# Kernel optimization log

Hardware: AMD Instinct MI355X
Metric: run time of the kernel (lower is better)

The kernel has to match this reference:

```python
import jax, jax.numpy as jnp
import numpy as np

ALPHA = 0.2  # LeakyReLU slope
NEG_INF = -9e15


def setup_inputs() -> dict:
    key = jax.random.key(0)
    ks = jax.random.split(key, 10)
    N, K, d = 20000, 32, 128
    R, S = 100, 4  # num relations, num domains
    item_embs = jax.random.normal(ks[0], (N, d), dtype=jnp.float32)
    entity_embs = jax.random.normal(ks[1], (N, K, d), dtype=jnp.float32)
    relations_embed = jax.random.normal(ks[2], (N, K, d), dtype=jnp.float32)
    relation_ids = jax.random.randint(ks[3], (N, K), 0, R, dtype=jnp.int32)
    adj_mask = jax.random.randint(ks[4], (N, K), 0, 2, dtype=jnp.int32)
    # fc_attention: Linear(3d, 1); out: Linear(d, d)
    fc_w = jax.random.normal(ks[5], (1, 3 * d), dtype=jnp.float32) * (1.0 / np.sqrt(3 * d))
    fc_b = jnp.zeros((1,), dtype=jnp.float32)
    out_w = jax.random.normal(ks[6], (d, d), dtype=jnp.float32) * (1.0 / np.sqrt(d))
    out_b = jnp.zeros((d,), dtype=jnp.float32)
    rel_dom_probs = jax.nn.softmax(jax.random.normal(ks[7], (R, S), dtype=jnp.float32), axis=-1)
    return {"item_embs": item_embs, "entity_embs": entity_embs,
            "relations_embed": relations_embed, "relation_ids": relation_ids,
            "adj_mask": adj_mask, "fc_w": fc_w, "fc_b": fc_b,
            "out_w": out_w, "out_b": out_b, "rel_dom_probs": rel_dom_probs}


def reference(item_embs, entity_embs, relations_embed, relation_ids, adj_mask,
              fc_w, fc_b, out_w, out_b, rel_dom_probs):
    N, K, d = entity_embs.shape
    R = rel_dom_probs.shape[0]
    # edge attention score: Linear(3d,1) on [item | relation | entity], then LeakyReLU
    Wh = jnp.broadcast_to(item_embs[:, None, :], (N, K, d))
    att_in = jnp.concatenate([Wh, relations_embed, entity_embs], axis=-1)  # [N,K,3d]
    e = jnp.einsum('nkf,of->nk', att_in, fc_w) + fc_b[0]
    e = jnp.where(e > 0, e, ALPHA * e)
    # masked softmax over neighbors (dropout inert in eval)
    masked = jnp.where(adj_mask > 0, e, NEG_INF)
    pi = jax.nn.softmax(masked, axis=1)  # [N,K]
    base = pi[..., None] * relations_embed * entity_embs  # [N,K,d]
    # domain-weighted aggregation: sum_s probs[rel_id, s], invalid ids -> 0
    valid = (relation_ids >= 0) & (relation_ids < R)
    safe_ids = jnp.clip(relation_ids, 0, R - 1)
    a_total = jnp.where(valid, rel_dom_probs[safe_ids].sum(-1), 0.0)  # [N,K]
    agg = jnp.einsum('nk,nkd->nd', a_total, base)  # [N,d]
    # residual + output Linear + ReLU
    out = (agg + item_embs) @ out_w.T + out_b
    return jax.nn.relu(out)
```

## Files before the change

kernel.cpp:

```cpp
#include <hip/hip_runtime.h>

#define ALPHA 0.2f

__device__ __forceinline__ float dot4(float4 a, float4 b) {
    return a.x * b.x + a.y * b.y + a.z * b.z + a.w * b.w;
}

__device__ __forceinline__ void block_bar() {
    asm volatile("s_waitcnt lgkmcnt(0)" ::: "memory");
    __builtin_amdgcn_s_barrier();
}

__global__ __launch_bounds__(256, 4)
void gat_k1(const float* __restrict__ item,
            const float* __restrict__ ent,
            const float* __restrict__ rel,
            const int*   __restrict__ rel_ids,
            const int*   __restrict__ adj,
            const float* __restrict__ fc_w,
            const float* __restrict__ fc_b,
            const float* __restrict__ probs,
            float* __restrict__ y,
            int N, int R)
{
    __shared__ float e_lds[32];
    __shared__ __align__(16) float part[4][128];
    __shared__ float asum[128];

    const int t  = threadIdx.x;
    const int w  = t >> 6;
    const int l  = t & 63;
    const int lh = l & 31;
    const int hi = l >> 5;
    const int kb = w * 8;

    for (int i = t; i < R; i += 256) {
        float4 q = *(const float4*)&probs[i * 4];
        asum[i] = q.x + q.y + q.z + q.w;
    }
    const float4 fi = *(const float4*)&fc_w[4 * lh];
    const float4 fr = *(const float4*)&fc_w[128 + 4 * lh];
    const float4 fe = *(const float4*)&fc_w[256 + 4 * lh];
    const float fcb = fc_b[0];
    __syncthreads();

    const int ST = gridDim.x;
    const int n0 = blockIdx.x;

    float4 rc[4], ec[4], itc;
    int adjc, idc;
    {
        const float* bR = rel + (size_t)n0 * 4096;
        const float* bE = ent + (size_t)n0 * 4096;
        #pragma unroll
        for (int c = 0; c < 4; ++c) {
            const int kk = kb + 2 * c + hi;
            rc[c] = *(const float4*)&bR[kk * 128 + 4 * lh];
            ec[c] = *(const float4*)&bE[kk * 128 + 4 * lh];
        }
        itc  = *(const float4*)&item[(size_t)n0 * 128 + 4 * lh];
        adjc = adj[(size_t)n0 * 32 + lh];
        idc  = rel_ids[(size_t)n0 * 32 + lh];
    }

    for (int n = n0; n < N; n += ST) {
        float4 p[4];
        float  ep[4];
        #pragma unroll
        for (int c = 0; c < 4; ++c) {
            p[c].x = rc[c].x * ec[c].x;
            p[c].y = rc[c].y * ec[c].y;
            p[c].z = rc[c].z * ec[c].z;
            p[c].w = rc[c].w * ec[c].w;
            ep[c]  = dot4(rc[c], fr) + dot4(ec[c], fe);
        }
        float sit = dot4(itc, fi);
        const float4 it_cur = itc;
        const int adj_cur = adjc, id_cur = idc;

        int np = n + ST; if (np >= N) np = n0;
        {
            const float* bR = rel + (size_t)np * 4096;
            const float* bE = ent + (size_t)np * 4096;
            #pragma unroll
            for (int c = 0; c < 4; ++c) {
                const int kk = kb + 2 * c + hi;
                rc[c] = *(const float4*)&bR[kk * 128 + 4 * lh];
                ec[c] = *(const float4*)&bE[kk * 128 + 4 * lh];
            }
            itc  = *(const float4*)&item[(size_t)np * 128 + 4 * lh];
            adjc = adj[(size_t)np * 32 + lh];
            idc  = rel_ids[(size_t)np * 32 + lh];
        }

        #pragma unroll
        for (int s = 16; s >= 1; s >>= 1) sit += __shfl_xor(sit, s, 32);
        #pragma unroll
        for (int c = 0; c < 4; ++c) {
            float v = ep[c];
            #pragma unroll
            for (int s = 16; s >= 1; s >>= 1) v += __shfl_xor(v, s, 32);
            ep[c] = v;
        }
        #pragma unroll
        for (int c = 0; c < 4; ++c)
            if (lh == c) e_lds[kb + 2 * c + hi] = ep[c];
        block_bar();

        float e = e_lds[lh] + sit + fcb;
        e = (e > 0.0f) ? e : ALPHA * e;
        float ex = (adj_cur > 0) ? __expf(e) : 0.0f;
        float Z = ex;
        #pragma unroll
        for (int s = 16; s >= 1; s >>= 1) Z += __shfl_xor(Z, s, 32);
        const bool  vld = (id_cur >= 0) && (id_cur < R);
        const float a   = vld ? asum[vld ? id_cur : 0] : 0.0f;
        const float wk  = (Z > 0.0f) ? (ex * a / Z) : (a * (1.0f / 32.0f));

        float4 acc = make_float4(0.f, 0.f, 0.f, 0.f);
        #pragma unroll
        for (int c = 0; c < 4; ++c) {
            const float wc = __shfl(wk, kb + 2 * c + hi, 32);
            acc.x = fmaf(wc, p[c].x, acc.x);
            acc.y = fmaf(wc, p[c].y, acc.y);
            acc.z = fmaf(wc, p[c].z, acc.z);
            acc.w = fmaf(wc, p[c].w, acc.w);
        }
        acc.x += __shfl_xor(acc.x, 32, 64);
        acc.y += __shfl_xor(acc.y, 32, 64);
        acc.z += __shfl_xor(acc.z, 32, 64);
        acc.w += __shfl_xor(acc.w, 32, 64);
        if (hi == 0) *(float4*)&part[w][4 * lh] = acc;
        block_bar();

        if (t < 32) {
            const float4 a0 = *(const float4*)&part[0][4 * t];
            const float4 a1 = *(const float4*)&part[1][4 * t];
            const float4 a2 = *(const float4*)&part[2][4 * t];
            const float4 a3 = *(const float4*)&part[3][4 * t];
            float4 o;
            o.x = a0.x + a1.x + a2.x + a3.x + it_cur.x;
            o.y = a0.y + a1.y + a2.y + a3.y + it_cur.y;
            o.z = a0.z + a1.z + a2.z + a3.z + it_cur.z;
            o.w = a0.w + a1.w + a2.w + a3.w + it_cur.w;
            *(float4*)&y[(size_t)n * 128 + 4 * t] = o;
        }
    }
}

__global__ __launch_bounds__(256, 4)
void gat_k2(const float* __restrict__ out_w,
            const float* __restrict__ out_b,
            float* __restrict__ y, int N)
{
    __shared__ __align__(16) float ylds[128];
    __shared__ __align__(16) float plds[1024];

    const int t = threadIdx.x;
    const int c = t & 7;
    const int g = t >> 3;

    float4 w4[16];
    #pragma unroll
    for (int a = 0; a < 4; ++a)
        #pragma unroll
        for (int i = 0; i < 4; ++i)
            w4[a * 4 + i] = *(const float4*)&out_w[(size_t)(g * 4 + a) * 128 + c * 16 + i * 4];
    const float bj = out_b[t & 127];
    const int stride = gridDim.x;

    float vcur = 0.0f;
    if (t < 128) vcur = y[(size_t)blockIdx.x * 128 + t];

    for (int n = blockIdx.x; n < N; n += stride) {
        if (t < 128) ylds[t] = vcur;
        block_bar();
        int np = n + stride; if (np >= N) np = n;
        float vn = 0.0f;
        if (t < 128) vn = y[(size_t)np * 128 + t];

        float4 yc[4];
        #pragma unroll
        for (int i = 0; i < 4; ++i) yc[i] = *(const float4*)&ylds[c * 16 + i * 4];
        #pragma unroll
        for (int a = 0; a < 4; ++a) {
            float s = 0.0f;
            #pragma unroll
            for (int i = 0; i < 4; ++i) s += dot4(w4[a * 4 + i], yc[i]);
            plds[a * 256 + g * 8 + c] = s;
        }
        block_bar();
        if (t < 128) {
            const int j = t, a2 = j & 3, g2 = j >> 2;
            const float* pp = &plds[a2 * 256 + g2 * 8];
            float4 u0 = *(const float4*)pp;
            float4 u1 = *(const float4*)(pp + 4);
            float s = u0.x + u0.y + u0.z + u0.w + u1.x + u1.y + u1.z + u1.w + bj;
            y[(size_t)n * 128 + j] = fmaxf(s, 0.0f);
        }
        vcur = vn;
    }
}

extern "C" void kernel_launch(void* const* d_in, const int* in_sizes, int n_in,
                              void* d_out, int out_size, void* d_ws, size_t ws_size,
                              hipStream_t stream) {
    const float* item    = (const float*)d_in[0];
    const float* ent     = (const float*)d_in[1];
    const float* rel     = (const float*)d_in[2];
    const int*   rel_ids = (const int*)  d_in[3];
    const int*   adj     = (const int*)  d_in[4];
    const float* fc_w    = (const float*)d_in[5];
    const float* fc_b    = (const float*)d_in[6];
    const float* out_w   = (const float*)d_in[7];
    const float* out_b   = (const float*)d_in[8];
    const float* probs   = (const float*)d_in[9];
    float* out = (float*)d_out;

    const int N = in_sizes[0] / 128;
    const int R = in_sizes[9] / 4;

    hipLaunchKernelGGL(gat_k1, dim3(2000), dim3(256), 0, stream,
                       item, ent, rel, rel_ids, adj, fc_w, fc_b, probs, out, N, R);

    int blocks2 = 2048; if (blocks2 > N) blocks2 = N;
    hipLaunchKernelGGL(gat_k2, dim3(blocks2), dim3(256), 0, stream,
                       out_w, out_b, out, N);
}
```

Before: 159.8 us.

## Fuse output linear layer into aggregation kernel with register-resident weights

Merges the two kernels into one. The aggregated row stays in LDS and is multiplied immediately by out_w, which each thread keeps in registers (64 floats of its own output row). This removes the round-trip of the intermediate y through global memory and one kernel launch. In exchange the grid shrinks from 2000 to 512 blocks and launch bounds drop to 2 blocks per SM, which lowers occupancy and latency hiding for a bandwidth-bound stream over the entity and relation tensors.

```diff
diff --git a/kernel.cpp b/kernel.cpp
--- a/kernel.cpp
+++ b/kernel.cpp
@@ -11,20 +11,23 @@
     __builtin_amdgcn_s_barrier();
 }
 
-__global__ __launch_bounds__(256, 4)
-void gat_k1(const float* __restrict__ item,
-            const float* __restrict__ ent,
-            const float* __restrict__ rel,
-            const int*   __restrict__ rel_ids,
-            const int*   __restrict__ adj,
-            const float* __restrict__ fc_w,
-            const float* __restrict__ fc_b,
-            const float* __restrict__ probs,
-            float* __restrict__ y,
-            int N, int R)
+__global__ __launch_bounds__(256, 2)
+void gat_fused(const float* __restrict__ item,
+               const float* __restrict__ ent,
+               const float* __restrict__ rel,
+               const int*   __restrict__ rel_ids,
+               const int*   __restrict__ adj,
+               const float* __restrict__ fc_w,
+               const float* __restrict__ fc_b,
+               const float* __restrict__ out_w,
+               const float* __restrict__ out_b,
+               const float* __restrict__ probs,
+               float* __restrict__ out,
+               int N, int R)
 {
     __shared__ float e_lds[32];
     __shared__ __align__(16) float part[4][128];
+    __shared__ __align__(16) float ylds[128];
     __shared__ float asum[128];
 
     const int t  = threadIdx.x;
@@ -42,6 +45,15 @@
     const float4 fr = *(const float4*)&fc_w[128 + 4 * lh];
     const float4 fe = *(const float4*)&fc_w[256 + 4 * lh];
     const float fcb = fc_b[0];
+
+    const int j = w * 32 + lh;
+    float4 w64[16];
+    {
+        const float* wrow = out_w + (size_t)j * 128 + hi * 64;
+        #pragma unroll
+        for (int i = 0; i < 16; ++i) w64[i] = *(const float4*)&wrow[4 * i];
+    }
+    const float bj = out_b[j];
     __syncthreads();
 
     const int ST = gridDim.x;
@@ -114,7 +126,7 @@
         #pragma unroll
         for (int s = 16; s >= 1; s >>= 1) Z += __shfl_xor(Z, s, 32);
         const bool  vld = (id_cur >= 0) && (id_cur < R);
-        const float a   = vld ? asum[vld ? id_cur : 0] : 0.0f;
+        const float a   = vld ? asum[id_cur] : 0.0f;
         const float wk  = (Z > 0.0f) ? (ex * a / Z) : (a * (1.0f / 32.0f));
 
         float4 acc = make_float4(0.f, 0.f, 0.f, 0.f);
@@ -143,62 +155,19 @@
             o.y = a0.y + a1.y + a2.y + a3.y + it_cur.y;
             o.z = a0.z + a1.z + a2.z + a3.z + it_cur.z;
             o.w = a0.w + a1.w + a2.w + a3.w + it_cur.w;
-            *(float4*)&y[(size_t)n * 128 + 4 * t] = o;
-        }
-    }
-}
-
-__global__ __launch_bounds__(256, 4)
-void gat_k2(const float* __restrict__ out_w,
-            const float* __restrict__ out_b,
-            float* __restrict__ y, int N)
-{
-    __shared__ __align__(16) float ylds[128];
-    __shared__ __align__(16) float plds[1024];
-
-    const int t = threadIdx.x;
-    const int c = t & 7;
-    const int g = t >> 3;
-
-    float4 w4[16];
-    #pragma unroll
-    for (int a = 0; a < 4; ++a)
-        #pragma unroll
-        for (int i = 0; i < 4; ++i)
-            w4[a * 4 + i] = *(const float4*)&out_w[(size_t)(g * 4 + a) * 128 + c * 16 + i * 4];
-    const float bj = out_b[t & 127];
-    const int stride = gridDim.x;
-
-    float vcur = 0.0f;
-    if (t < 128) vcur = y[(size_t)blockIdx.x * 128 + t];
-
-    for (int n = blockIdx.x; n < N; n += stride) {
-        if (t < 128) ylds[t] = vcur;
-        block_bar();
-        int np = n + stride; if (np >= N) np = n;
-        float vn = 0.0f;
-        if (t < 128) vn = y[(size_t)np * 128 + t];
-
-        float4 yc[4];
-        #pragma unroll
-        for (int i = 0; i < 4; ++i) yc[i] = *(const float4*)&ylds[c * 16 + i * 4];
-        #pragma unroll
-        for (int a = 0; a < 4; ++a) {
-            float s = 0.0f;
-            #pragma unroll
-            for (int i = 0; i < 4; ++i) s += dot4(w4[a * 4 + i], yc[i]);
-            plds[a * 256 + g * 8 + c] = s;
+            *(float4*)&ylds[4 * t] = o;
         }
         block_bar();
-        if (t < 128) {
-            const int j = t, a2 = j & 3, g2 = j >> 2;
-            const float* pp = &plds[a2 * 256 + g2 * 8];
-            float4 u0 = *(const float4*)pp;
-            float4 u1 = *(const float4*)(pp + 4);
-            float s = u0.x + u0.y + u0.z + u0.w + u1.x + u1.y + u1.z + u1.w + bj;
-            y[(size_t)n * 128 + j] = fmaxf(s, 0.0f);
+
+        float s = 0.0f;
+        #pragma unroll
+        for (int i = 0; i < 16; ++i) {
+            const float4 yv = *(const float4*)&ylds[hi * 64 + 4 * i];
+            s += dot4(w64[i], yv);
         }
-        vcur = vn;
+        s += __shfl_xor(s, 32, 64);
+        if (hi == 0)
+            out[(size_t)n * 128 + j] = fmaxf(s + bj, 0.0f);
     }
 }
 
@@ -220,10 +189,7 @@
     const int N = in_sizes[0] / 128;
     const int R = in_sizes[9] / 4;
 
-    hipLaunchKernelGGL(gat_k1, dim3(2000), dim3(256), 0, stream,
-                       item, ent, rel, rel_ids, adj, fc_w, fc_b, probs, out, N, R);
-
-    int blocks2 = 2048; if (blocks2 > N) blocks2 = N;
-    hipLaunchKernelGGL(gat_k2, dim3(blocks2), dim3(256), 0, stream,
-                       out_w, out_b, out, N);
+    hipLaunchKernelGGL(gat_fused, dim3(512), dim3(256), 0, stream,
+                       item, ent, rel, rel_ids, adj, fc_w, fc_b,
+                       out_w, out_b, probs, out, N, R);
 }
```

New measurement: 140.6 us. 12.0% less time.
